# Performance work log

Measured on AMD Instinct MI355X. Metric: run time of the kernel, lower is better.

The kernel has to match this reference:

```python
import jax, jax.numpy as jnp
import numpy as np
import math

NUM_CLASSES = 722
BLUR_RANGE = 3
# gaussian_val(dist, sigma=1) = exp(-2**dist / (2 * 2**1)) = exp(-2**dist / 4)
DECAYS = [math.exp(-(2.0 ** d) / 4.0) for d in range(BLUR_RANGE + 1)]


def setup_inputs() -> dict:
    key = jax.random.key(0)
    k1, k2 = jax.random.split(key)
    pred = jax.random.normal(k1, (32, 2048, NUM_CLASSES), dtype=jnp.float32)
    target = jax.random.randint(k2, (32, 2048), 0, NUM_CLASSES, dtype=jnp.int32)
    return {"pred": pred, "target": target}


def _smoothed_label(target):
    # target: (b, t) int -> (b, t, C) float32 gaussian-blurred one-hot.
    b, t = target.shape
    bi = jnp.arange(b)[:, None]   # (b, 1)
    ti = jnp.arange(t)[None, :]   # (1, t)
    one_hot = jnp.zeros((b, t, NUM_CLASSES), dtype=jnp.float32)
    # Same scatter order as the torch loop: dist = blur..0, direction +1 then -1;
    # later (smaller-dist) scatters overwrite earlier ones, incl. clamped indices.
    for dist in range(BLUR_RANGE, -1, -1):
        for direction in (1, -1):
            blur_idx = jnp.clip(target + direction * dist, 0, NUM_CLASSES - 1)
            one_hot = one_hot.at[bi, ti, blur_idx].set(DECAYS[dist])
    # to_onehot: exact target position gets 1.0 (overwrites decay[0]).
    one_hot = one_hot.at[bi, ti, target].set(1.0)
    return one_hot


def reference(pred, target):
    # pred: (b, t, C) logits; target: (b, t) class indices.
    pred_logit = jax.nn.log_softmax(pred, axis=-1)
    target_smoothed = _smoothed_label(target)
    target_loss_sum = jnp.sum(-pred_logit * target_smoothed, axis=-1)  # (b, t)
    return jnp.mean(target_loss_sum)
```

## Files before the change

kernel.cpp:

```cpp
#include <hip/hip_runtime.h>
#include <math.h>

#define NC 722
#define NF2 361
#define NROWS 65536
#define ROWS_PER_WAVE 4
#define WAVES_PER_BLOCK 4
#define ROWS_PER_BLOCK (ROWS_PER_WAVE * WAVES_PER_BLOCK)

__global__ void init_out_kernel(float* out) {
    if (threadIdx.x == 0) out[0] = 0.0f;
}

__global__ __launch_bounds__(256) void ce_gauss_kernel(
        const float* __restrict__ pred,
        const int* __restrict__ target,
        float* __restrict__ out) {
    const int lane = threadIdx.x & 63;
    const int wave = threadIdx.x >> 6;
    __shared__ float wt_lds[WAVES_PER_BLOCK][ROWS_PER_WAVE][8];
    __shared__ float wave_sums[WAVES_PER_BLOCK];

    const int row0 = blockIdx.x * ROWS_PER_BLOCK + wave * ROWS_PER_WAVE;

    int   tgt[ROWS_PER_WAVE];
    float sumw[ROWS_PER_WAVE];
    const float DEC1 = 0.606530659713f;
    const float DEC2 = 0.367879441171f;
    const float DEC3 = 0.135335283237f;
    #pragma unroll
    for (int rr = 0; rr < ROWS_PER_WAVE; ++rr) {
        const int t = target[row0 + rr];
        tgt[rr] = t;
        float w[7] = {0.f, 0.f, 0.f, 0.f, 0.f, 0.f, 0.f};
        #pragma unroll
        for (int dist = 3; dist >= 1; --dist) {
            const float dv = (dist == 3) ? DEC3 : (dist == 2) ? DEC2 : DEC1;
            int ip = t + dist; if (ip > NC - 1) ip = NC - 1;
            int im = t - dist; if (im < 0) im = 0;
            w[ip - t + 3] = dv;
            w[im - t + 3] = dv;
        }
        w[3] = 1.0f;
        sumw[rr] = w[0] + w[1] + w[2] + w[3] + w[4] + w[5] + w[6];
        if (lane == 0) {
            #pragma unroll
            for (int j = 0; j < 7; ++j) wt_lds[wave][rr][j] = w[j];
        }
    }

    const float2* __restrict__ p2[ROWS_PER_WAVE];
    #pragma unroll
    for (int rr = 0; rr < ROWS_PER_WAVE; ++rr)
        p2[rr] = (const float2*)(pred + (size_t)(row0 + rr) * NC);

    float se[ROWS_PER_WAVE] = {0.f, 0.f, 0.f, 0.f};
    #pragma unroll
    for (int k = 0; k < 6; ++k) {
        const int idx = lane + (k << 6);
        if (idx < NF2) {
            float2 v0 = p2[0][idx];
            float2 v1 = p2[1][idx];
            float2 v2 = p2[2][idx];
            float2 v3 = p2[3][idx];
            se[0] += __expf(v0.x) + __expf(v0.y);
            se[1] += __expf(v1.x) + __expf(v1.y);
            se[2] += __expf(v2.x) + __expf(v2.y);
            se[3] += __expf(v3.x) + __expf(v3.y);
        }
    }
    #pragma unroll
    for (int rr = 0; rr < ROWS_PER_WAVE; ++rr) {
        #pragma unroll
        for (int off = 32; off > 0; off >>= 1)
            se[rr] += __shfl_xor(se[rr], off, 64);
    }

    float dotv = 0.f;
    const int grr = lane >> 3;
    const int gj  = lane & 7;
    if (grr < ROWS_PER_WAVE && gj < 7) {
        const float wv = wt_lds[wave][grr][gj];
        if (wv > 0.f) {
            const int c = tgt[grr] - 3 + gj;
            dotv = wv * pred[(size_t)(row0 + grr) * NC + c];
        }
    }
    dotv += __shfl_xor(dotv, 1, 64);
    dotv += __shfl_xor(dotv, 2, 64);
    dotv += __shfl_xor(dotv, 4, 64);

    float acc = 0.f;
    if (gj == 0 && grr < ROWS_PER_WAVE)
        acc = sumw[grr] * __logf(se[grr]) - dotv;
    #pragma unroll
    for (int off = 32; off > 0; off >>= 1)
        acc += __shfl_xor(acc, off, 64);

    if (lane == 0) wave_sums[wave] = acc;
    __syncthreads();
    if (threadIdx.x == 0) {
        float s = wave_sums[0] + wave_sums[1] + wave_sums[2] + wave_sums[3];
        atomicAdd(out, s * (1.0f / (float)NROWS));
    }
}

extern "C" void kernel_launch(void* const* d_in, const int* in_sizes, int n_in,
                              void* d_out, int out_size, void* d_ws, size_t ws_size,
                              hipStream_t stream) {
    const float* pred = (const float*)d_in[0];
    const int* target = (const int*)d_in[1];
    float* out = (float*)d_out;

    init_out_kernel<<<1, 64, 0, stream>>>(out);

    const int grid = NROWS / ROWS_PER_BLOCK;
    ce_gauss_kernel<<<grid, 256, 0, stream>>>(pred, target, out);
}
```

Measured before the change: 270.5 us.

## Process row pairs with float4 loads and 8 rows per wave

Each wave now handles 8 rows, read as 4 contiguous row pairs. Each lane loads float4 chunks that may straddle the two rows of a pair, and the sum is split by chunk index. This is meant to widen memory transactions and add more loads in flight per wave, and the grid is halved. Target weights, the sum of weights and the per-row exp sums now go through LDS so all 64 lanes can use them in the gather phase. The change adds register pressure from 8 accumulators and branchy selects in the hot loop.

```diff
diff --git a/kernel.cpp b/kernel.cpp
--- a/kernel.cpp
+++ b/kernel.cpp
@@ -2,11 +2,12 @@
 #include <math.h>
 
 #define NC 722
-#define NF2 361
 #define NROWS 65536
-#define ROWS_PER_WAVE 4
+#define PAIRS_PER_WAVE 4
+#define ROWS_PER_WAVE 8
 #define WAVES_PER_BLOCK 4
-#define ROWS_PER_BLOCK (ROWS_PER_WAVE * WAVES_PER_BLOCK)
+#define ROWS_PER_BLOCK 32
+#define NF4 361
 
 __global__ void init_out_kernel(float* out) {
     if (threadIdx.x == 0) out[0] = 0.0f;
@@ -18,72 +19,84 @@
         float* __restrict__ out) {
     const int lane = threadIdx.x & 63;
     const int wave = threadIdx.x >> 6;
-    __shared__ float wt_lds[WAVES_PER_BLOCK][ROWS_PER_WAVE][8];
+
+    __shared__ float wt_lds[WAVES_PER_BLOCK][ROWS_PER_WAVE * 8];
+    __shared__ float se_lds[WAVES_PER_BLOCK][ROWS_PER_WAVE];
+    __shared__ int   tg_lds[WAVES_PER_BLOCK][ROWS_PER_WAVE];
     __shared__ float wave_sums[WAVES_PER_BLOCK];
 
     const int row0 = blockIdx.x * ROWS_PER_BLOCK + wave * ROWS_PER_WAVE;
 
-    int   tgt[ROWS_PER_WAVE];
-    float sumw[ROWS_PER_WAVE];
-    const float DEC1 = 0.606530659713f;
-    const float DEC2 = 0.367879441171f;
-    const float DEC3 = 0.135335283237f;
+    const float4* __restrict__ p4[PAIRS_PER_WAVE];
     #pragma unroll
-    for (int rr = 0; rr < ROWS_PER_WAVE; ++rr) {
-        const int t = target[row0 + rr];
-        tgt[rr] = t;
-        float w[7] = {0.f, 0.f, 0.f, 0.f, 0.f, 0.f, 0.f};
-        #pragma unroll
-        for (int dist = 3; dist >= 1; --dist) {
-            const float dv = (dist == 3) ? DEC3 : (dist == 2) ? DEC2 : DEC1;
-            int ip = t + dist; if (ip > NC - 1) ip = NC - 1;
-            int im = t - dist; if (im < 0) im = 0;
-            w[ip - t + 3] = dv;
-            w[im - t + 3] = dv;
-        }
-        w[3] = 1.0f;
-        sumw[rr] = w[0] + w[1] + w[2] + w[3] + w[4] + w[5] + w[6];
-        if (lane == 0) {
+    for (int p = 0; p < PAIRS_PER_WAVE; ++p)
+        p4[p] = (const float4*)(pred + (size_t)(row0 + 2 * p) * NC);
+
+    float se[ROWS_PER_WAVE] = {0.f, 0.f, 0.f, 0.f, 0.f, 0.f, 0.f, 0.f};
+    #pragma unroll
+    for (int k = 0; k < 6; ++k) {
+        const int g = lane + (k << 6);
+        if (g < NF4) {
+            const bool aE = (g < 180);
+            const bool aO = (g > 180);
             #pragma unroll
-            for (int j = 0; j < 7; ++j) wt_lds[wave][rr][j] = w[j];
+            for (int p = 0; p < PAIRS_PER_WAVE; ++p) {
+                float4 v = p4[p][g];
+                float e0 = __expf(v.x), e1 = __expf(v.y);
+                float e2 = __expf(v.z), e3 = __expf(v.w);
+                float s01 = e0 + e1, s23 = e2 + e3, s4 = s01 + s23;
+                se[2 * p]     += aE ? s4 : (aO ? 0.f : s01);
+                se[2 * p + 1] += aO ? s4 : (aE ? 0.f : s23);
+            }
         }
     }
 
-    const float2* __restrict__ p2[ROWS_PER_WAVE];
-    #pragma unroll
-    for (int rr = 0; rr < ROWS_PER_WAVE; ++rr)
-        p2[rr] = (const float2*)(pred + (size_t)(row0 + rr) * NC);
-
-    float se[ROWS_PER_WAVE] = {0.f, 0.f, 0.f, 0.f};
-    #pragma unroll
-    for (int k = 0; k < 6; ++k) {
-        const int idx = lane + (k << 6);
-        if (idx < NF2) {
-            float2 v0 = p2[0][idx];
-            float2 v1 = p2[1][idx];
-            float2 v2 = p2[2][idx];
-            float2 v3 = p2[3][idx];
-            se[0] += __expf(v0.x) + __expf(v0.y);
-            se[1] += __expf(v1.x) + __expf(v1.y);
-            se[2] += __expf(v2.x) + __expf(v2.y);
-            se[3] += __expf(v3.x) + __expf(v3.y);
+    {
+        const float DEC1 = 0.606530659713f;
+        const float DEC2 = 0.367879441171f;
+        const float DEC3 = 0.135335283237f;
+        #pragma unroll
+        for (int rr = 0; rr < ROWS_PER_WAVE; ++rr) {
+            const int t = target[row0 + rr];
+            float w[7] = {0.f, 0.f, 0.f, 0.f, 0.f, 0.f, 0.f};
+            #pragma unroll
+            for (int dist = 3; dist >= 1; --dist) {
+                const float dv = (dist == 3) ? DEC3 : (dist == 2) ? DEC2 : DEC1;
+                int ip = t + dist; if (ip > NC - 1) ip = NC - 1;
+                int im = t - dist; if (im < 0) im = 0;
+                w[ip - t + 3] = dv;
+                w[im - t + 3] = dv;
+            }
+            w[3] = 1.0f;
+            const float sw = w[0] + w[1] + w[2] + w[3] + w[4] + w[5] + w[6];
+            if (lane == 0) {
+                #pragma unroll
+                for (int j = 0; j < 7; ++j) wt_lds[wave][rr * 8 + j] = w[j];
+                wt_lds[wave][rr * 8 + 7] = sw;
+                tg_lds[wave][rr] = t;
+            }
         }
     }
+
     #pragma unroll
     for (int rr = 0; rr < ROWS_PER_WAVE; ++rr) {
         #pragma unroll
         for (int off = 32; off > 0; off >>= 1)
             se[rr] += __shfl_xor(se[rr], off, 64);
     }
+    if (lane == 0) {
+        #pragma unroll
+        for (int rr = 0; rr < ROWS_PER_WAVE; ++rr) se_lds[wave][rr] = se[rr];
+    }
 
-    float dotv = 0.f;
     const int grr = lane >> 3;
     const int gj  = lane & 7;
-    if (grr < ROWS_PER_WAVE && gj < 7) {
-        const float wv = wt_lds[wave][grr][gj];
+    const int t   = tg_lds[wave][grr];
+    float dotv = 0.f;
+    if (gj < 7) {
+        const float wv = wt_lds[wave][grr * 8 + gj];
         if (wv > 0.f) {
-            const int c = tgt[grr] - 3 + gj;
-            dotv = wv * pred[(size_t)(row0 + grr) * NC + c];
+            dotv = wv * pred[(size_t)(row0 + grr) * NC + (t - 3 + gj)];
         }
     }
     dotv += __shfl_xor(dotv, 1, 64);
@@ -91,8 +104,11 @@
     dotv += __shfl_xor(dotv, 4, 64);
 
     float acc = 0.f;
-    if (gj == 0 && grr < ROWS_PER_WAVE)
-        acc = sumw[grr] * __logf(se[grr]) - dotv;
+    if (gj == 0) {
+        const float sw  = wt_lds[wave][grr * 8 + 7];
+        const float sev = se_lds[wave][grr];
+        acc = sw * __logf(sev) - dotv;
+    }
     #pragma unroll
     for (int off = 32; off > 0; off >>= 1)
         acc += __shfl_xor(acc, off, 64);
```

New measurement: 286.3 us. 5.9% more time.
